# Performance work log

Hardware: AMD Instinct MI355X
Metric: run time of the kernel (lower is better)

Reference implementation:

```python
import jax, jax.numpy as jnp
import numpy as np

T, B, H = 1024, 16, 1024
S = 2048


def setup_inputs() -> dict:
    key = jax.random.key(0)
    k1, k2, k3, k4 = jax.random.split(key, 4)
    output = jax.random.normal(k1, (T, B, H), dtype=jnp.float32)
    memory = jax.random.normal(k2, (S, B, H), dtype=jnp.float32)
    attn_mask = jnp.zeros((B, T, S), dtype=jnp.bool_)  # True = masked
    # linear_out: Linear(2H -> H); torch weight layout [out, in]
    W = jax.random.normal(k3, (H, 2 * H), dtype=jnp.float32) * (1.0 / np.sqrt(2 * H))
    b = jax.random.normal(k4, (H,), dtype=jnp.float32) * 0.01
    return {"output": output, "memory": memory, "attn_mask": attn_mask, "W": W, "b": b}


def reference(output, memory, attn_mask, W, b):
    # scores: (B, T, S) = output^T @ memory (unscaled dot product)
    attn = jnp.einsum('tbh,sbh->bts', output, memory)
    attn = jnp.where(attn_mask, -jnp.inf, attn)
    attn = jax.nn.softmax(attn, axis=2)
    # context: (T, B, H)
    context = jnp.einsum('bts,sbh->tbh', attn, memory)
    combined = jnp.concatenate([context, output], axis=2)  # (T, B, 2H)
    out = jnp.tanh(jnp.einsum('tbd,hd->tbh', combined, W) + b)
    return (out, attn)
```

## Files before the change

kernel.cpp:

```cpp
#include <hip/hip_runtime.h>
#include <hip/hip_bf16.h>
#include <math.h>

#define Tn 1024
#define Bn 16
#define Hn 1024
#define Sn 2048
#define LDP 40

typedef __attribute__((ext_vector_type(8))) short bf16x8;
typedef __attribute__((ext_vector_type(8))) unsigned short u16x8;
typedef __attribute__((ext_vector_type(4))) float f32x4;

__device__ __forceinline__ unsigned short f2bf(float x) {
  unsigned u = __float_as_uint(x);
  u += 0x7fffu + ((u >> 16) & 1u);
  return (unsigned short)(u >> 16);
}
__device__ __forceinline__ float bf2f(unsigned short h) {
  return __uint_as_float(((unsigned)h) << 16);
}
__device__ __forceinline__ void split2(float x, unsigned short& hi, unsigned short& lo) {
  hi = f2bf(x);
  lo = f2bf(x - bf2f(hi));
}

__device__ __forceinline__ void gload16(const void* g, void* l) {
  __builtin_amdgcn_global_load_lds((const __attribute__((address_space(1))) void*)g,
                                   (__attribute__((address_space(3))) void*)l, 16, 0, 0);
}


__global__ __launch_bounds__(256) void k_cvt8(const float* __restrict__ src,
                                              unsigned short* __restrict__ dst, int n8) {
  const int i = blockIdx.x * 256 + threadIdx.x;
  if (i >= n8) return;
  const float4 a = *(const float4*)(src + (size_t)i * 8);
  const float4 c = *(const float4*)(src + (size_t)i * 8 + 4);
  u16x8 u;
  u[0] = f2bf(a.x); u[1] = f2bf(a.y); u[2] = f2bf(a.z); u[3] = f2bf(a.w);
  u[4] = f2bf(c.x); u[5] = f2bf(c.y); u[6] = f2bf(c.z); u[7] = f2bf(c.w);
  *(u16x8*)(dst + (size_t)i * 8) = u;
}

__global__ __launch_bounds__(256) void k_tr_mem(const float* __restrict__ mem,
                                                unsigned short* __restrict__ memT) {
  __shared__ unsigned short L[64 * 72];
  const int t = threadIdx.x;
  const int h0 = blockIdx.x * 64, s0 = blockIdx.y * 64, b = blockIdx.z;
#pragma unroll
  for (int p = 0; p < 4; ++p) {
    const int fid = p * 256 + t;
    const int s_l = fid >> 4;
    const int h_l = (fid & 15) * 4;
    const float4 v = *(const float4*)(mem + ((size_t)(s0 + s_l) * Bn + b) * Hn + h0 + h_l);
    unsigned short e[4] = {f2bf(v.x), f2bf(v.y), f2bf(v.z), f2bf(v.w)};
#pragma unroll
    for (int i0 = 0; i0 < 4; ++i0) {
      const int i = (i0 + (t & 3)) & 3;
      L[(h_l + i) * 72 + s_l] = e[i];
    }
  }
  __syncthreads();
#pragma unroll
  for (int p = 0; p < 2; ++p) {
    const int cid = p * 256 + t;
    const int h_l = cid >> 3;
    const int c = cid & 7;
    const bf16x8 vv = *(const bf16x8*)&L[h_l * 72 + c * 8];
    *(bf16x8*)(memT + ((size_t)b * Hn + h0 + h_l) * Sn + s0 + c * 8) = vv;
  }
}


__device__ __forceinline__ void stage_rows(const float* __restrict__ g, size_t ldr,
                                           unsigned short* __restrict__ Lhi,
                                           unsigned short* __restrict__ Llo, int tid) {
#pragma unroll
  for (int it = 0; it < 4; ++it) {
    const int r = (tid >> 3) + it * 32;
    const int c = (tid & 7) * 4;
    const float4 v = *(const float4*)(g + (size_t)r * ldr + c);
    unsigned short h0, h1, h2, h3, l0, l1, l2, l3;
    split2(v.x, h0, l0); split2(v.y, h1, l1); split2(v.z, h2, l2); split2(v.w, h3, l3);
    uint2 hp, lp;
    hp.x = (unsigned)h0 | ((unsigned)h1 << 16);
    hp.y = (unsigned)h2 | ((unsigned)h3 << 16);
    lp.x = (unsigned)l0 | ((unsigned)l1 << 16);
    lp.y = (unsigned)l2 | ((unsigned)l3 << 16);
    *(uint2*)&Lhi[r * LDP + c] = hp;
    *(uint2*)&Llo[r * LDP + c] = lp;
  }
}

__device__ __forceinline__ void mfma_tile(const unsigned short* __restrict__ Ah,
                                          const unsigned short* __restrict__ Al,
                                          const unsigned short* __restrict__ Bh,
                                          const unsigned short* __restrict__ Bl,
                                          int wm, int wn, int lane, f32x4 (&acc)[4][4]) {
  const int r16 = lane & 15;
  const int kh = (lane >> 4) * 8;
  bf16x8 ah[4], al[4], bh[4], bl[4];
#pragma unroll
  for (int i = 0; i < 4; ++i) {
    const int off = (wm + i * 16 + r16) * LDP + kh;
    ah[i] = *(const bf16x8*)&Ah[off];
    al[i] = *(const bf16x8*)&Al[off];
  }
#pragma unroll
  for (int j = 0; j < 4; ++j) {
    const int off = (wn + j * 16 + r16) * LDP + kh;
    bh[j] = *(const bf16x8*)&Bh[off];
    bl[j] = *(const bf16x8*)&Bl[off];
  }
#pragma unroll
  for (int i = 0; i < 4; ++i)
#pragma unroll
    for (int j = 0; j < 4; ++j) {
      acc[i][j] = __builtin_amdgcn_mfma_f32_16x16x32_bf16(ah[i], bh[j], acc[i][j], 0, 0, 0);
      acc[i][j] = __builtin_amdgcn_mfma_f32_16x16x32_bf16(ah[i], bl[j], acc[i][j], 0, 0, 0);
      acc[i][j] = __builtin_amdgcn_mfma_f32_16x16x32_bf16(al[i], bh[j], acc[i][j], 0, 0, 0);
    }
}

__global__ __launch_bounds__(256, 2) void k_scores(const float* __restrict__ outp,
                                                   const float* __restrict__ mem,
                                                   float* __restrict__ attn) {
  __shared__ unsigned short Ah[128 * LDP], Al[128 * LDP], Bh[128 * LDP], Bl[128 * LDP];
  const int tid = threadIdx.x;
  const int lane = tid & 63;
  const int wv = tid >> 6;
  const int wm = (wv >> 1) * 64, wn = (wv & 1) * 64;
  const int bs = blockIdx.x * 128;
  const int bt = blockIdx.y * 128;
  const int b = blockIdx.z;
  const f32x4 fz = {0.f, 0.f, 0.f, 0.f};
  f32x4 acc[4][4];
#pragma unroll
  for (int i = 0; i < 4; ++i)
#pragma unroll
    for (int j = 0; j < 4; ++j) acc[i][j] = fz;

  const float* Ag = outp + ((size_t)bt * Bn + b) * Hn;
  const float* Bg = mem + ((size_t)bs * Bn + b) * Hn;
  for (int k0 = 0; k0 < Hn; k0 += 32) {
    stage_rows(Ag + k0, (size_t)Bn * Hn, Ah, Al, tid);
    stage_rows(Bg + k0, (size_t)Bn * Hn, Bh, Bl, tid);
    __syncthreads();
    mfma_tile(Ah, Al, Bh, Bl, wm, wn, lane, acc);
    __syncthreads();
  }
  const int r16 = lane & 15;
  const int rq = (lane >> 4) * 4;
  float* obase = attn + (size_t)b * Tn * Sn;
#pragma unroll
  for (int i = 0; i < 4; ++i)
#pragma unroll
    for (int q = 0; q < 4; ++q) {
      const int t = bt + wm + i * 16 + rq + q;
#pragma unroll
      for (int j = 0; j < 4; ++j) {
        const int s = bs + wn + j * 16 + r16;
        obase[(size_t)t * Sn + s] = acc[i][j][q];
      }
    }
}


__global__ __launch_bounds__(256) void k_softmax(float* __restrict__ attn,
                                                 const unsigned char* __restrict__ mask,
                                                 unsigned short* __restrict__ attnbf) {
  const int row = blockIdx.x;
  float* p = attn + (size_t)row * Sn;
  const unsigned char* mrow = mask + (size_t)row * Sn;
  const int tid = threadIdx.x;
  const int lane = tid & 63;
  const int wv = tid >> 6;
  const float4 a = *(const float4*)(p + tid * 8);
  const float4 c = *(const float4*)(p + tid * 8 + 4);
  const unsigned long long mv = *(const unsigned long long*)(mrow + tid * 8);
  float x[8] = {a.x, a.y, a.z, a.w, c.x, c.y, c.z, c.w};
#pragma unroll
  for (int j = 0; j < 8; ++j)
    if ((mv >> (8 * j)) & 0xffull) x[j] = -INFINITY;
  float mx = x[0];
#pragma unroll
  for (int j = 1; j < 8; ++j) mx = fmaxf(mx, x[j]);
#pragma unroll
  for (int off = 32; off; off >>= 1) mx = fmaxf(mx, __shfl_xor(mx, off, 64));
  __shared__ float redmax[4], redsum[4];
  if (lane == 0) redmax[wv] = mx;
  __syncthreads();
  mx = fmaxf(fmaxf(redmax[0], redmax[1]), fmaxf(redmax[2], redmax[3]));
  float e[8];
  float s = 0.f;
#pragma unroll
  for (int j = 0; j < 8; ++j) {
    e[j] = __expf(x[j] - mx);
    s += e[j];
  }
#pragma unroll
  for (int off = 32; off; off >>= 1) s += __shfl_xor(s, off, 64);
  if (lane == 0) redsum[wv] = s;
  __syncthreads();
  s = redsum[0] + redsum[1] + redsum[2] + redsum[3];
  const float inv = 1.0f / s;
  float o[8];
#pragma unroll
  for (int j = 0; j < 8; ++j) o[j] = e[j] * inv;
  float4 o0 = {o[0], o[1], o[2], o[3]};
  float4 o1 = {o[4], o[5], o[6], o[7]};
  *(float4*)(p + tid * 8) = o0;
  *(float4*)(p + tid * 8 + 4) = o1;
  u16x8 ub;
#pragma unroll
  for (int j = 0; j < 8; ++j) ub[j] = f2bf(o[j]);
  *(u16x8*)(attnbf + (size_t)row * Sn + tid * 8) = ub;
}


__device__ __forceinline__ void stage128x64(const unsigned short* __restrict__ g, size_t ldr,
                                            unsigned short* __restrict__ lds, int tid) {
  const int wv = tid >> 6;
  const int row = tid >> 3;
  const size_t coff = (size_t)(tid & 7) * 8;
#pragma unroll
  for (int q = 0; q < 4; ++q) {
    gload16(g + (size_t)(q * 32 + row) * ldr + coff, lds + q * 2048 + wv * 512);
  }
}

__device__ __forceinline__ void mfma64(const unsigned short* __restrict__ A,
                                       const unsigned short* __restrict__ B,
                                       int wm, int wn, int lane, f32x4 (&acc)[4][4]) {
  const int r16 = lane & 15;
  const int kh = (lane >> 4) * 8;
#pragma unroll
  for (int ks = 0; ks < 2; ++ks) {
    bf16x8 a[4], bb[4];
#pragma unroll
    for (int i = 0; i < 4; ++i) a[i] = *(const bf16x8*)&A[(wm + i * 16 + r16) * 64 + ks * 32 + kh];
#pragma unroll
    for (int j = 0; j < 4; ++j) bb[j] = *(const bf16x8*)&B[(wn + j * 16 + r16) * 64 + ks * 32 + kh];
#pragma unroll
    for (int i = 0; i < 4; ++i)
#pragma unroll
      for (int j = 0; j < 4; ++j)
        acc[i][j] = __builtin_amdgcn_mfma_f32_16x16x32_bf16(a[i], bb[j], acc[i][j], 0, 0, 0);
  }
}

__global__ __launch_bounds__(256, 3) void k_context(const unsigned short* __restrict__ attnbf,
                                                    const unsigned short* __restrict__ memT,
                                                    unsigned short* __restrict__ ctxbf) {
  __shared__ unsigned short As[128 * 64], Bs[128 * 64];
  const int tid = threadIdx.x, lane = tid & 63, wv = tid >> 6;
  const int wm = (wv >> 1) * 64, wn = (wv & 1) * 64;
  const int bh = blockIdx.x * 128, bt = blockIdx.y * 128, b = blockIdx.z;
  const f32x4 fz = {0.f, 0.f, 0.f, 0.f};
  f32x4 acc[4][4];
#pragma unroll
  for (int i = 0; i < 4; ++i)
#pragma unroll
    for (int j = 0; j < 4; ++j) acc[i][j] = fz;

  const unsigned short* Ag = attnbf + ((size_t)b * Tn + bt) * Sn;
  const unsigned short* Bg = memT + ((size_t)b * Hn + bh) * Sn;
  for (int k0 = 0; k0 < Sn; k0 += 64) {
    stage128x64(Ag + k0, Sn, As, tid);
    stage128x64(Bg + k0, Sn, Bs, tid);
    __syncthreads();
    mfma64(As, Bs, wm, wn, lane, acc);
    __syncthreads();
  }
  const int r16 = lane & 15, rq = (lane >> 4) * 4;
#pragma unroll
  for (int i = 0; i < 4; ++i)
#pragma unroll
    for (int q = 0; q < 4; ++q) {
      const int t = bt + wm + i * 16 + rq + q;
#pragma unroll
      for (int j = 0; j < 4; ++j) {
        const int h = bh + wn + j * 16 + r16;
        ctxbf[((size_t)t * Bn + b) * Hn + h] = f2bf(acc[i][j][q]);
      }
    }
}

__global__ __launch_bounds__(256, 3) void k_final(const unsigned short* __restrict__ ctxbf,
                                                  const unsigned short* __restrict__ outpbf,
                                                  const unsigned short* __restrict__ Wbf,
                                                  const float* __restrict__ bias,
                                                  float* __restrict__ out) {
  __shared__ unsigned short As[128 * 64], Bs[128 * 64];
  const int tid = threadIdx.x, lane = tid & 63, wv = tid >> 6;
  const int wm = (wv >> 1) * 64, wn = (wv & 1) * 64;
  const int bh = blockIdx.x * 128, bm = blockIdx.y * 128;
  const f32x4 fz = {0.f, 0.f, 0.f, 0.f};
  f32x4 acc[4][4];
#pragma unroll
  for (int i = 0; i < 4; ++i)
#pragma unroll
    for (int j = 0; j < 4; ++j) acc[i][j] = fz;

  for (int k0 = 0; k0 < 2 * Hn; k0 += 64) {
    const unsigned short* Ag = (k0 < Hn) ? (ctxbf + (size_t)bm * Hn + k0)
                                         : (outpbf + (size_t)bm * Hn + (k0 - Hn));
    stage128x64(Ag, Hn, As, tid);
    stage128x64(Wbf + (size_t)bh * (2 * Hn) + k0, 2 * Hn, Bs, tid);
    __syncthreads();
    mfma64(As, Bs, wm, wn, lane, acc);
    __syncthreads();
  }
  const int r16 = lane & 15, rq = (lane >> 4) * 4;
  float bj[4];
#pragma unroll
  for (int j = 0; j < 4; ++j) bj[j] = bias[bh + wn + j * 16 + r16];
#pragma unroll
  for (int i = 0; i < 4; ++i)
#pragma unroll
    for (int q = 0; q < 4; ++q) {
      const int r = bm + wm + i * 16 + rq + q;
#pragma unroll
      for (int j = 0; j < 4; ++j) {
        const int h = bh + wn + j * 16 + r16;
        out[(size_t)r * Hn + h] = tanhf(acc[i][j][q] + bj[j]);
      }
    }
}

extern "C" void kernel_launch(void* const* d_in, const int* in_sizes, int n_in,
                              void* d_out, int out_size, void* d_ws, size_t ws_size,
                              hipStream_t stream) {
  const float* outp = (const float*)d_in[0];
  const float* mem = (const float*)d_in[1];
  const unsigned char* mask = (const unsigned char*)d_in[2];
  const float* W = (const float*)d_in[3];
  const float* bias = (const float*)d_in[4];
  float* out = (float*)d_out;
  float* attn = out + (size_t)Tn * Bn * Hn;

  char* w = (char*)d_ws;
  unsigned short* memT = (unsigned short*)w;
  unsigned short* attnbf = (unsigned short*)(w + (size_t)67108864);
  unsigned short* ctxbf = (unsigned short*)(w + (size_t)134217728);
  unsigned short* outpbf = (unsigned short*)(w + (size_t)167772160);
  unsigned short* Wbf = (unsigned short*)(w + (size_t)201326592);

  k_cvt8<<<dim3((Tn * Bn * Hn / 8) / 256), 256, 0, stream>>>(outp, outpbf, Tn * Bn * Hn / 8);
  k_cvt8<<<dim3((Hn * 2 * Hn / 8) / 256), 256, 0, stream>>>(W, Wbf, Hn * 2 * Hn / 8);
  k_tr_mem<<<dim3(Hn / 64, Sn / 64, Bn), 256, 0, stream>>>(mem, memT);

  k_scores<<<dim3(Sn / 128, Tn / 128, Bn), 256, 0, stream>>>(outp, mem, attn);
  k_softmax<<<dim3(Bn * Tn), 256, 0, stream>>>(attn, mask, attnbf);
  k_context<<<dim3(Hn / 128, Tn / 128, Bn), 256, 0, stream>>>(attnbf, memT, ctxbf);
  k_final<<<dim3(Hn / 128, (Tn * Bn) / 128), 256, 0, stream>>>(ctxbf, outpbf, Wbf, bias, out);
}
```

Baseline: 629.3 us.

## Pre-split inputs into batch-major bf16 hi/lo planes and stage scores via direct LDS loads

Adds a pre-pass that splits output and memory into bf16 hi/lo planes stored batch-major ([B][rows][H]). The scores GEMM can then stream contiguous bf16 tiles with global_load_lds instead of reading strided fp32 rows and doing the split conversion inside the main loop. The memory transpose now reads the bf16 hi plane. Workspace buffers are reused (memL becomes memT, memH becomes attnbf, outpL becomes ctx), and the final GEMM writes its output back in the original [T][B][H] layout. The cost is an extra full pass over both inputs plus larger intermediate traffic. Buffer aliasing also depends on kernel ordering being correct.

New measurement: 565.9 us. -10.1%, faster.

```diff
diff --git a/kernel.cpp b/kernel.cpp
--- a/kernel.cpp
+++ b/kernel.cpp
@@ -6,7 +6,6 @@
 #define Bn 16
 #define Hn 1024
 #define Sn 2048
-#define LDP 40
 
 typedef __attribute__((ext_vector_type(8))) short bf16x8;
 typedef __attribute__((ext_vector_type(8))) unsigned short u16x8;
@@ -20,16 +19,36 @@
 __device__ __forceinline__ float bf2f(unsigned short h) {
   return __uint_as_float(((unsigned)h) << 16);
 }
-__device__ __forceinline__ void split2(float x, unsigned short& hi, unsigned short& lo) {
-  hi = f2bf(x);
-  lo = f2bf(x - bf2f(hi));
-}
 
 __device__ __forceinline__ void gload16(const void* g, void* l) {
   __builtin_amdgcn_global_load_lds((const __attribute__((address_space(1))) void*)g,
                                    (__attribute__((address_space(3))) void*)l, 16, 0, 0);
 }
 
+
+__global__ __launch_bounds__(256) void k_split_plane(const float* __restrict__ src,
+                                                     unsigned short* __restrict__ hiP,
+                                                     unsigned short* __restrict__ loP,
+                                                     int rows) {
+  const int i = blockIdx.x * 256 + threadIdx.x;
+  const int h8 = i & (Hn / 8 - 1);
+  const int rem = i >> 7;
+  const int b = rem & (Bn - 1);
+  const int r = rem >> 4;
+  const float4 a = *(const float4*)(src + (size_t)i * 8);
+  const float4 c = *(const float4*)(src + (size_t)i * 8 + 4);
+  const float v[8] = {a.x, a.y, a.z, a.w, c.x, c.y, c.z, c.w};
+  u16x8 hv, lv;
+#pragma unroll
+  for (int j = 0; j < 8; ++j) {
+    const unsigned short h = f2bf(v[j]);
+    hv[j] = h;
+    lv[j] = f2bf(v[j] - bf2f(h));
+  }
+  const size_t dst = ((size_t)b * rows + r) * Hn + h8 * 8;
+  *(u16x8*)(hiP + dst) = hv;
+  *(u16x8*)(loP + dst) = lv;
+}
 
 __global__ __launch_bounds__(256) void k_cvt8(const float* __restrict__ src,
                                               unsigned short* __restrict__ dst, int n8) {
@@ -43,23 +62,19 @@
   *(u16x8*)(dst + (size_t)i * 8) = u;
 }
 
-__global__ __launch_bounds__(256) void k_tr_mem(const float* __restrict__ mem,
-                                                unsigned short* __restrict__ memT) {
+__global__ __launch_bounds__(256) void k_trH(const unsigned short* __restrict__ memH,
+                                             unsigned short* __restrict__ memT) {
   __shared__ unsigned short L[64 * 72];
   const int t = threadIdx.x;
   const int h0 = blockIdx.x * 64, s0 = blockIdx.y * 64, b = blockIdx.z;
 #pragma unroll
-  for (int p = 0; p < 4; ++p) {
+  for (int p = 0; p < 2; ++p) {
     const int fid = p * 256 + t;
-    const int s_l = fid >> 4;
-    const int h_l = (fid & 15) * 4;
-    const float4 v = *(const float4*)(mem + ((size_t)(s0 + s_l) * Bn + b) * Hn + h0 + h_l);
-    unsigned short e[4] = {f2bf(v.x), f2bf(v.y), f2bf(v.z), f2bf(v.w)};
-#pragma unroll
-    for (int i0 = 0; i0 < 4; ++i0) {
-      const int i = (i0 + (t & 3)) & 3;
-      L[(h_l + i) * 72 + s_l] = e[i];
-    }
+    const int s_l = fid >> 3;
+    const int c = fid & 7;
+    const u16x8 v = *(const u16x8*)(memH + ((size_t)b * Sn + s0 + s_l) * Hn + h0 + c * 8);
+#pragma unroll
+    for (int e = 0; e < 8; ++e) L[(c * 8 + e) * 72 + s_l] = v[e];
   }
   __syncthreads();
 #pragma unroll
@@ -67,73 +82,42 @@
     const int cid = p * 256 + t;
     const int h_l = cid >> 3;
     const int c = cid & 7;
-    const bf16x8 vv = *(const bf16x8*)&L[h_l * 72 + c * 8];
-    *(bf16x8*)(memT + ((size_t)b * Hn + h0 + h_l) * Sn + s0 + c * 8) = vv;
-  }
-}
-
-
-__device__ __forceinline__ void stage_rows(const float* __restrict__ g, size_t ldr,
-                                           unsigned short* __restrict__ Lhi,
-                                           unsigned short* __restrict__ Llo, int tid) {
-#pragma unroll
-  for (int it = 0; it < 4; ++it) {
-    const int r = (tid >> 3) + it * 32;
-    const int c = (tid & 7) * 4;
-    const float4 v = *(const float4*)(g + (size_t)r * ldr + c);
-    unsigned short h0, h1, h2, h3, l0, l1, l2, l3;
-    split2(v.x, h0, l0); split2(v.y, h1, l1); split2(v.z, h2, l2); split2(v.w, h3, l3);
-    uint2 hp, lp;
-    hp.x = (unsigned)h0 | ((unsigned)h1 << 16);
-    hp.y = (unsigned)h2 | ((unsigned)h3 << 16);
-    lp.x = (unsigned)l0 | ((unsigned)l1 << 16);
-    lp.y = (unsigned)l2 | ((unsigned)l3 << 16);
-    *(uint2*)&Lhi[r * LDP + c] = hp;
-    *(uint2*)&Llo[r * LDP + c] = lp;
-  }
-}
-
-__device__ __forceinline__ void mfma_tile(const unsigned short* __restrict__ Ah,
-                                          const unsigned short* __restrict__ Al,
-                                          const unsigned short* __restrict__ Bh,
-                                          const unsigned short* __restrict__ Bl,
-                                          int wm, int wn, int lane, f32x4 (&acc)[4][4]) {
-  const int r16 = lane & 15;
-  const int kh = (lane >> 4) * 8;
-  bf16x8 ah[4], al[4], bh[4], bl[4];
-#pragma unroll
-  for (int i = 0; i < 4; ++i) {
-    const int off = (wm + i * 16 + r16) * LDP + kh;
-    ah[i] = *(const bf16x8*)&Ah[off];
-    al[i] = *(const bf16x8*)&Al[off];
-  }
-#pragma unroll
-  for (int j = 0; j < 4; ++j) {
-    const int off = (wn + j * 16 + r16) * LDP + kh;
-    bh[j] = *(const bf16x8*)&Bh[off];
-    bl[j] = *(const bf16x8*)&Bl[off];
-  }
-#pragma unroll
-  for (int i = 0; i < 4; ++i)
-#pragma unroll
-    for (int j = 0; j < 4; ++j) {
-      acc[i][j] = __builtin_amdgcn_mfma_f32_16x16x32_bf16(ah[i], bh[j], acc[i][j], 0, 0, 0);
-      acc[i][j] = __builtin_amdgcn_mfma_f32_16x16x32_bf16(ah[i], bl[j], acc[i][j], 0, 0, 0);
-      acc[i][j] = __builtin_amdgcn_mfma_f32_16x16x32_bf16(al[i], bh[j], acc[i][j], 0, 0, 0);
-    }
-}
-
-__global__ __launch_bounds__(256, 2) void k_scores(const float* __restrict__ outp,
-                                                   const float* __restrict__ mem,
+    const u16x8 vv = *(const u16x8*)&L[h_l * 72 + c * 8];
+    *(u16x8*)(memT + ((size_t)b * Hn + h0 + h_l) * Sn + s0 + c * 8) = vv;
+  }
+}
+
+
+__device__ __forceinline__ void stage128x32(const unsigned short* __restrict__ g, size_t ldr,
+                                            unsigned short* __restrict__ lds, int tid) {
+  const int wv = tid >> 6;
+  const int row = tid >> 2;
+  const size_t coff = (size_t)(tid & 3) * 8;
+#pragma unroll
+  for (int q = 0; q < 2; ++q)
+    gload16(g + (size_t)(q * 64 + row) * ldr + coff, lds + q * 2048 + wv * 512);
+}
+
+__device__ __forceinline__ void stage128x64(const unsigned short* __restrict__ g, size_t ldr,
+                                            unsigned short* __restrict__ lds, int tid) {
+  const int wv = tid >> 6;
+  const int row = tid >> 3;
+  const size_t coff = (size_t)(tid & 7) * 8;
+#pragma unroll
+  for (int q = 0; q < 4; ++q)
+    gload16(g + (size_t)(q * 32 + row) * ldr + coff, lds + q * 2048 + wv * 512);
+}
+
+
+__global__ __launch_bounds__(256, 3) void k_scores(const unsigned short* __restrict__ oH,
+                                                   const unsigned short* __restrict__ oL,
+                                                   const unsigned short* __restrict__ mH,
+                                                   const unsigned short* __restrict__ mL,
                                                    float* __restrict__ attn) {
-  __shared__ unsigned short Ah[128 * LDP], Al[128 * LDP], Bh[128 * LDP], Bl[128 * LDP];
-  const int tid = threadIdx.x;
-  const int lane = tid & 63;
-  const int wv = tid >> 6;
+  __shared__ unsigned short AsH[128 * 32], AsL[128 * 32], BsH[128 * 32], BsL[128 * 32];
+  const int tid = threadIdx.x, lane = tid & 63, wv = tid >> 6;
   const int wm = (wv >> 1) * 64, wn = (wv & 1) * 64;
-  const int bs = blockIdx.x * 128;
-  const int bt = blockIdx.y * 128;
-  const int b = blockIdx.z;
+  const int bs = blockIdx.x * 128, bt = blockIdx.y * 128, b = blockIdx.z;
   const f32x4 fz = {0.f, 0.f, 0.f, 0.f};
   f32x4 acc[4][4];
 #pragma unroll
@@ -141,16 +125,36 @@
 #pragma unroll
     for (int j = 0; j < 4; ++j) acc[i][j] = fz;
 
-  const float* Ag = outp + ((size_t)bt * Bn + b) * Hn;
-  const float* Bg = mem + ((size_t)bs * Bn + b) * Hn;
+  const unsigned short* AgH = oH + ((size_t)b * Tn + bt) * Hn;
+  const unsigned short* AgL = oL + ((size_t)b * Tn + bt) * Hn;
+  const unsigned short* BgH = mH + ((size_t)b * Sn + bs) * Hn;
+  const unsigned short* BgL = mL + ((size_t)b * Sn + bs) * Hn;
+  const int r16 = lane & 15, kh = (lane >> 4) * 8;
   for (int k0 = 0; k0 < Hn; k0 += 32) {
-    stage_rows(Ag + k0, (size_t)Bn * Hn, Ah, Al, tid);
-    stage_rows(Bg + k0, (size_t)Bn * Hn, Bh, Bl, tid);
-    __syncthreads();
-    mfma_tile(Ah, Al, Bh, Bl, wm, wn, lane, acc);
-    __syncthreads();
-  }
-  const int r16 = lane & 15;
+    stage128x32(AgH + k0, Hn, AsH, tid);
+    stage128x32(AgL + k0, Hn, AsL, tid);
+    stage128x32(BgH + k0, Hn, BsH, tid);
+    stage128x32(BgL + k0, Hn, BsL, tid);
+    __syncthreads();
+    bf16x8 ah[4], al[4];
+#pragma unroll
+    for (int i = 0; i < 4; ++i) {
+      ah[i] = *(const bf16x8*)&AsH[(wm + i * 16 + r16) * 32 + kh];
+      al[i] = *(const bf16x8*)&AsL[(wm + i * 16 + r16) * 32 + kh];
+    }
+#pragma unroll
+    for (int j = 0; j < 4; ++j) {
+      const bf16x8 bh = *(const bf16x8*)&BsH[(wn + j * 16 + r16) * 32 + kh];
+      const bf16x8 bl = *(const bf16x8*)&BsL[(wn + j * 16 + r16) * 32 + kh];
+#pragma unroll
+      for (int i = 0; i < 4; ++i) {
+        acc[i][j] = __builtin_amdgcn_mfma_f32_16x16x32_bf16(ah[i], bh, acc[i][j], 0, 0, 0);
+        acc[i][j] = __builtin_amdgcn_mfma_f32_16x16x32_bf16(ah[i], bl, acc[i][j], 0, 0, 0);
+        acc[i][j] = __builtin_amdgcn_mfma_f32_16x16x32_bf16(al[i], bh, acc[i][j], 0, 0, 0);
+      }
+    }
+    __syncthreads();
+  }
   const int rq = (lane >> 4) * 4;
   float* obase = attn + (size_t)b * Tn * Sn;
 #pragma unroll
@@ -219,17 +223,6 @@
 }
 
 
-__device__ __forceinline__ void stage128x64(const unsigned short* __restrict__ g, size_t ldr,
-                                            unsigned short* __restrict__ lds, int tid) {
-  const int wv = tid >> 6;
-  const int row = tid >> 3;
-  const size_t coff = (size_t)(tid & 7) * 8;
-#pragma unroll
-  for (int q = 0; q < 4; ++q) {
-    gload16(g + (size_t)(q * 32 + row) * ldr + coff, lds + q * 2048 + wv * 512);
-  }
-}
-
 __device__ __forceinline__ void mfma64(const unsigned short* __restrict__ A,
                                        const unsigned short* __restrict__ B,
                                        int wm, int wn, int lane, f32x4 (&acc)[4][4]) {
@@ -252,7 +245,7 @@
 
 __global__ __launch_bounds__(256, 3) void k_context(const unsigned short* __restrict__ attnbf,
                                                     const unsigned short* __restrict__ memT,
-                                                    unsigned short* __restrict__ ctxbf) {
+                                                    unsigned short* __restrict__ ctxB) {
   __shared__ unsigned short As[128 * 64], Bs[128 * 64];
   const int tid = threadIdx.x, lane = tid & 63, wv = tid >> 6;
   const int wm = (wv >> 1) * 64, wn = (wv & 1) * 64;
@@ -282,13 +275,13 @@
 #pragma unroll
       for (int j = 0; j < 4; ++j) {
         const int h = bh + wn + j * 16 + r16;
-        ctxbf[((size_t)t * Bn + b) * Hn + h] = f2bf(acc[i][j][q]);
+        ctxB[((size_t)b * Tn + t) * Hn + h] = f2bf(acc[i][j][q]);
       }
     }
 }
 
-__global__ __launch_bounds__(256, 3) void k_final(const unsigned short* __restrict__ ctxbf,
-                                                  const unsigned short* __restrict__ outpbf,
+__global__ __launch_bounds__(256, 3) void k_final(const unsigned short* __restrict__ ctxB,
+                                                  const unsigned short* __restrict__ outpH,
                                                   const unsigned short* __restrict__ Wbf,
                                                   const float* __restrict__ bias,
                                                   float* __restrict__ out) {
@@ -304,8 +297,8 @@
     for (int j = 0; j < 4; ++j) acc[i][j] = fz;
 
   for (int k0 = 0; k0 < 2 * Hn; k0 += 64) {
-    const unsigned short* Ag = (k0 < Hn) ? (ctxbf + (size_t)bm * Hn + k0)
-                                         : (outpbf + (size_t)bm * Hn + (k0 - Hn));
+    const unsigned short* Ag = (k0 < Hn) ? (ctxB + (size_t)bm * Hn + k0)
+                                         : (outpH + (size_t)bm * Hn + (k0 - Hn));
     stage128x64(Ag, Hn, As, tid);
     stage128x64(Wbf + (size_t)bh * (2 * Hn) + k0, 2 * Hn, Bs, tid);
     __syncthreads();
@@ -321,10 +314,11 @@
 #pragma unroll
     for (int q = 0; q < 4; ++q) {
       const int r = bm + wm + i * 16 + rq + q;
+      const int b = r >> 10, t = r & (Tn - 1);
 #pragma unroll
       for (int j = 0; j < 4; ++j) {
         const int h = bh + wn + j * 16 + r16;
-        out[(size_t)r * Hn + h] = tanhf(acc[i][j][q] + bj[j]);
+        out[((size_t)t * Bn + b) * Hn + h] = tanhf(acc[i][j][q] + bj[j]);
       }
     }
 }
@@ -341,18 +335,22 @@
   float* attn = out + (size_t)Tn * Bn * Hn;
 
   char* w = (char*)d_ws;
-  unsigned short* memT = (unsigned short*)w;
-  unsigned short* attnbf = (unsigned short*)(w + (size_t)67108864);
-  unsigned short* ctxbf = (unsigned short*)(w + (size_t)134217728);
-  unsigned short* outpbf = (unsigned short*)(w + (size_t)167772160);
-  unsigned short* Wbf = (unsigned short*)(w + (size_t)201326592);
-
-  k_cvt8<<<dim3((Tn * Bn * Hn / 8) / 256), 256, 0, stream>>>(outp, outpbf, Tn * Bn * Hn / 8);
+  unsigned short* memH  = (unsigned short*)(w);
+  unsigned short* memL  = (unsigned short*)(w + ((size_t)64 << 20));
+  unsigned short* outpH = (unsigned short*)(w + ((size_t)128 << 20));
+  unsigned short* outpL = (unsigned short*)(w + ((size_t)160 << 20));
+  unsigned short* Wbf   = (unsigned short*)(w + ((size_t)192 << 20));
+  unsigned short* memT   = memL;
+  unsigned short* attnbf = memH;
+  unsigned short* ctxB   = outpL;
+
+  k_split_plane<<<dim3((Tn * Bn * Hn / 8) / 256), 256, 0, stream>>>(outp, outpH, outpL, Tn);
+  k_split_plane<<<dim3((Sn * Bn * Hn / 8) / 256), 256, 0, stream>>>(mem, memH, memL, Sn);
   k_cvt8<<<dim3((Hn * 2 * Hn / 8) / 256), 256, 0, stream>>>(W, Wbf, Hn * 2 * Hn / 8);
-  k_tr_mem<<<dim3(Hn / 64, Sn / 64, Bn), 256, 0, stream>>>(mem, memT);
-
-  k_scores<<<dim3(Sn / 128, Tn / 128, Bn), 256, 0, stream>>>(outp, mem, attn);
+
+  k_scores<<<dim3(Sn / 128, Tn / 128, Bn), 256, 0, stream>>>(outpH, outpL, memH, memL, attn);
+  k_trH<<<dim3(Hn / 64, Sn / 64, Bn), 256, 0, stream>>>(memH, memT);
   k_softmax<<<dim3(Bn * Tn), 256, 0, stream>>>(attn, mask, attnbf);
-  k_context<<<dim3(Hn / 128, Tn / 128, Bn), 256, 0, stream>>>(attnbf, memT, ctxbf);
-  k_final<<<dim3(Hn / 128, (Tn * Bn) / 128), 256, 0, stream>>>(ctxbf, outpbf, Wbf, bias, out);
-}
+  k_context<<<dim3(Hn / 128, Tn / 128, Bn), 256, 0, stream>>>(attnbf, memT, ctxB);
+  k_final<<<dim3(Hn / 128, (Tn * Bn) / 128), 256, 0, stream>>>(ctxB, outpH, Wbf, bias, out);
+}
```
